# Performance work log

Measured on AMD Instinct MI355X. Metric: run time of the kernel, lower is better.

Reference implementation:

```python
import jax, jax.numpy as jnp
import numpy as np

RADIUS2 = 0.03 ** 2
SIM_THRESH = 0.7
EPS = 1e-8


def setup_inputs() -> dict:
    key = jax.random.key(0)
    k1, k2, k3, k4, k5, k6, k7 = jax.random.split(key, 7)
    B, N, D = 2, 6144, 32
    # points in a 0.3-side cube so radius 0.03 gives realistic neighbor counts
    points = jax.random.uniform(k1, (B, N, 3), dtype=jnp.float32) * 0.3
    embeddings = jax.random.normal(k2, (B, N, D), dtype=jnp.float32)
    leaf_mask = jax.random.randint(k3, (B, N), 0, 2, dtype=jnp.int32)
    # consistency_net: Linear(2D, D) -> ReLU -> Linear(D, D)
    W1 = jax.random.normal(k4, (2 * D, D), dtype=jnp.float32) * (1.0 / np.sqrt(2 * D))
    b1 = jax.random.normal(k5, (D,), dtype=jnp.float32) * 0.01
    W2 = jax.random.normal(k6, (D, D), dtype=jnp.float32) * (1.0 / np.sqrt(D))
    b2 = jax.random.normal(k7, (D,), dtype=jnp.float32) * 0.01
    return {"points": points, "embeddings": embeddings, "leaf_mask": leaf_mask,
            "W1": W1, "b1": b1, "W2": W2, "b2": b2}


def reference(points, embeddings, leaf_mask, W1, b1, W2, b2):
    # points: [B,N,3], embeddings: [B,N,D], leaf_mask: [B,N] int (0/1)
    dt = embeddings.dtype
    leaf = leaf_mask > 0  # [B,N] bool

    # pairwise squared distances via the Gram trick (avoids [B,N,N,3])
    pn = jnp.sum(points * points, axis=-1)                      # [B,N]
    gram = jnp.einsum('bic,bjc->bij', points, points)           # [B,N,N]
    d2 = jnp.maximum(pn[:, :, None] + pn[:, None, :] - 2.0 * gram, 0.0)

    # neighbor mask: within radius AND neighbor is leaf (matches dist<0.03 & leaf_mask)
    nb = (d2 < RADIUS2) & leaf[:, None, :]                      # [B,N,N]

    # cosine similarity with torch's eps clamp on norms
    enorm = jnp.maximum(jnp.linalg.norm(embeddings, axis=-1), EPS)  # [B,N]
    inner = jnp.einsum('bid,bjd->bij', embeddings, embeddings)      # [B,N,N]
    sims = inner / (enorm[:, :, None] * enorm[:, None, :])

    sim_mask = nb & (sims > SIM_THRESH)                          # [B,N,N]
    cnt_nb = jnp.sum(nb, axis=-1)                                # [B,N]
    cnt_sim = jnp.sum(sim_mask, axis=-1)                         # [B,N]

    # mean of similar-neighbor embeddings
    sum_sim = jnp.einsum('bij,bjd->bid', sim_mask.astype(dt), embeddings)
    mean_sim = sum_sim / jnp.maximum(cnt_sim, 1).astype(dt)[..., None]

    # consistency MLP on [center_embedding, mean_similar]
    combined = jnp.concatenate([embeddings, mean_sim], axis=-1)  # [B,N,2D]
    h = jax.nn.relu(jnp.einsum('bnk,kd->bnd', combined, W1) + b1)
    out = jnp.einsum('bnk,kd->bnd', h, W2) + b2                  # [B,N,D]

    # refine only leaf points with >1 neighbor and >0 similar neighbors
    cond = leaf & (cnt_nb > 1) & (cnt_sim > 0)                   # [B,N]
    refined = jnp.where(cond[..., None], out, embeddings)

    # per-batch early exit: sum(leaf_mask) < 10 -> unchanged
    batch_ok = jnp.sum(leaf_mask, axis=-1) >= 10                 # [B]
    return jnp.where(batch_ok[:, None, None], refined, embeddings)
```

## Files before the change

### kernel.cpp

```cpp
#include <hip/hip_runtime.h>

#define NPTS    6144
#define DIM     32
#define NB      2
#define NCELL   1000
#define R2      0.0009f
#define NWAVES  4
#define BLOCK   (NWAVES * 64)
#define LEAFBIT 8192
#define PPT     6
#define NBCAP   128

__device__ __forceinline__ int cellof(float x) {
    int c = (int)(x * (10.0f / 0.3f));
    return min(max(c, 0), 9);
}

#define WS_LEAF   0
#define WS_CSTART 4
#define WS_SORTED 2008

__global__ __launch_bounds__(1024)
void build_cells(const float* __restrict__ points, const int* __restrict__ leaf,
                 int* __restrict__ ws)
{
    __shared__ int s_hist[1024];
    __shared__ int s_cursor[1024];
    __shared__ int s_wsum[16];
    __shared__ int s_leaf;

    const int t = threadIdx.x;
    const int b = blockIdx.x;
    const int w = t >> 6, lane = t & 63;

    s_hist[t] = 0;
    if (t == 0) s_leaf = 0;

    float px[PPT], py[PPT], pz[PPT];
    int   pc[PPT], pw[PPT];

    __syncthreads();

    int lc = 0;
    #pragma unroll
    for (int r = 0; r < PPT; ++r) {
        const int i  = r * 1024 + t;
        const int gi = b * NPTS + i;
        px[r] = points[gi * 3 + 0];
        py[r] = points[gi * 3 + 1];
        pz[r] = points[gi * 3 + 2];
        const int lf = leaf[gi] > 0 ? 1 : 0;
        lc += lf;
        pc[r] = (cellof(pz[r]) * 10 + cellof(py[r])) * 10 + cellof(px[r]);
        pw[r] = i + (lf ? LEAFBIT : 0);
        atomicAdd(&s_hist[pc[r]], 1);
    }
    #pragma unroll
    for (int off = 32; off > 0; off >>= 1) lc += __shfl_down(lc, off);
    if (lane == 0) atomicAdd(&s_leaf, lc);
    __syncthreads();

    const int v = s_hist[t];
    int x = v;
    #pragma unroll
    for (int off = 1; off < 64; off <<= 1) {
        const int y = __shfl_up(x, off);
        if (lane >= off) x += y;
    }
    if (lane == 63) s_wsum[w] = x;
    __syncthreads();
    if (t < 16) {
        int wv = s_wsum[t];
        #pragma unroll
        for (int off = 1; off < 16; off <<= 1) {
            const int y = __shfl_up(wv, off);
            if (t >= off) wv += y;
        }
        s_wsum[t] = wv;
    }
    __syncthreads();
    const int incl = x + (w > 0 ? s_wsum[w - 1] : 0);
    s_cursor[t] = incl - v;

    if (t < NCELL) ws[WS_CSTART + b * (NCELL + 1) + t + 1] = incl;
    if (t == 0) {
        ws[WS_CSTART + b * (NCELL + 1)] = 0;
        ws[WS_LEAF + b] = s_leaf;
    }
    __syncthreads();

    float4* sorted = (float4*)(ws + WS_SORTED) + (size_t)b * NPTS;
    #pragma unroll
    for (int r = 0; r < PPT; ++r) {
        const int pos = atomicAdd(&s_cursor[pc[r]], 1);
        sorted[pos] = make_float4(px[r], py[r], pz[r], (float)pw[r]);
    }
}

__global__ __launch_bounds__(BLOCK)
void refine(const float* __restrict__ emb,
            const float* __restrict__ W1, const float* __restrict__ b1,
            const float* __restrict__ W2, const float* __restrict__ b2,
            const int* __restrict__ ws, float* __restrict__ out)
{
    __shared__ __align__(16) float s_ei[NWAVES][DIM];
    __shared__ float s_mean[NWAVES][DIM];
    __shared__ float s_h[NWAVES][DIM];
    __shared__ int   s_nb[NWAVES][NBCAP];
    __shared__ int   s_sv[NWAVES][NBCAP];

    const int tid  = threadIdx.x;
    const int wid  = tid >> 6;
    const int lane = tid & 63;
    const int s    = blockIdx.x * NWAVES + wid;
    const int b    = s / NPTS;
    const int slot = s - b * NPTS;

    const float4* srt  = (const float4*)(ws + WS_SORTED) + (size_t)b * NPTS;
    const int*    cst  = ws + WS_CSTART + b * (NCELL + 1);
    const float*  embB = emb + (size_t)b * NPTS * DIM;

    const float4 P  = srt[slot];
    const int    iw = (int)P.w;
    const int    io = iw & (LEAFBIT - 1);
    const bool   li = (iw & LEAFBIT) != 0;
    const bool   ok = ws[WS_LEAF + b] >= 10;

    const float4* e4   = (const float4*)(embB + (size_t)io * DIM);
    float4*       out4 = (float4*)(out + ((size_t)b * NPTS + io) * DIM);

    if (!(ok && li)) {
        if (lane < DIM / 4) out4[lane] = e4[lane];
        return;
    }

    if (lane < DIM) s_ei[wid][lane] = ((const float*)e4)[lane];

    float ni2 = 0.0f;
    #pragma unroll
    for (int d = 0; d < DIM; ++d) { const float v = s_ei[wid][d]; ni2 += v * v; }
    const float rni = 1.0f / fmaxf(sqrtf(ni2), 1e-8f);

    const int cx = cellof(P.x), cy = cellof(P.y), cz = cellof(P.z);

    int begv = 0, lenv = 0;
    if (lane < 9) {
        const int z = cz + lane / 3 - 1;
        const int y = cy + lane % 3 - 1;
        if ((unsigned)z <= 9u && (unsigned)y <= 9u) {
            const int rowb = (z * 10 + y) * 10;
            const int c0   = rowb + max(cx - 1, 0);
            const int c1   = rowb + min(cx + 1, 9);
            begv = cst[c0];
            lenv = cst[c1 + 1] - begv;
        }
    }
    const int rb0 = __shfl(begv, 0), rb1 = __shfl(begv, 1), rb2 = __shfl(begv, 2);
    const int rb3 = __shfl(begv, 3), rb4 = __shfl(begv, 4), rb5 = __shfl(begv, 5);
    const int rb6 = __shfl(begv, 6), rb7 = __shfl(begv, 7), rb8 = __shfl(begv, 8);
    const int ln0 = __shfl(lenv, 0), ln1 = __shfl(lenv, 1), ln2 = __shfl(lenv, 2);
    const int ln3 = __shfl(lenv, 3), ln4 = __shfl(lenv, 4), ln5 = __shfl(lenv, 5);
    const int ln6 = __shfl(lenv, 6), ln7 = __shfl(lenv, 7), ln8 = __shfl(lenv, 8);
    const int pf1 = ln0,       pf2 = pf1 + ln1, pf3 = pf2 + ln2;
    const int pf4 = pf3 + ln3, pf5 = pf4 + ln4, pf6 = pf5 + ln5;
    const int pf7 = pf6 + ln6, pf8 = pf7 + ln7, pf9 = pf8 + ln8;

    int nbcnt = 0;
    for (int base = 0; base < pf9; base += 64) {
        const int g = base + lane;
        int j = 0;
        if (g < pf9) j = rb8 + g - pf8;
        if (g < pf8) j = rb7 + g - pf7;
        if (g < pf7) j = rb6 + g - pf6;
        if (g < pf6) j = rb5 + g - pf5;
        if (g < pf5) j = rb4 + g - pf4;
        if (g < pf4) j = rb3 + g - pf3;
        if (g < pf3) j = rb2 + g - pf2;
        if (g < pf2) j = rb1 + g - pf1;
        if (g < pf1) j = rb0 + g;
        const float4 Q  = srt[j];
        const float dx = Q.x - P.x, dy = Q.y - P.y, dz = Q.z - P.z;
        const float d2 = dx * dx + dy * dy + dz * dz;
        const int   jw = (int)Q.w;
        const bool  nb = (g < pf9) && (d2 < R2) && ((jw & LEAFBIT) != 0);
        const unsigned long long m = __ballot(nb);
        if (nb) {
            const int pos = nbcnt + __popcll(m & ((1ull << lane) - 1ull));
            if (pos < NBCAP) s_nb[wid][pos] = jw & (LEAFBIT - 1);
        }
        nbcnt += __popcll(m);
    }
    const int cnt_nb = nbcnt;

    int csim = 0;
    const int nh = min(cnt_nb, NBCAP);
    for (int h0 = 0; h0 < nh; h0 += 64) {
        const int h = h0 + lane;
        bool surv = false;
        int  jo   = 0;
        if (h < nh) {
            jo = s_nb[wid][h];
            const float4* ej4 = (const float4*)(embB + (size_t)jo * DIM);
            float dot = 0.0f, nj2 = 0.0f;
            #pragma unroll
            for (int k = 0; k < DIM / 4; ++k) {
                const float4 v = ej4[k];
                const float4 a = *(const float4*)&s_ei[wid][4 * k];
                dot += a.x * v.x + a.y * v.y + a.z * v.z + a.w * v.w;
                nj2 += v.x * v.x + v.y * v.y + v.z * v.z + v.w * v.w;
            }
            const float rnj = 1.0f / fmaxf(sqrtf(nj2), 1e-8f);
            surv = (dot * rni * rnj) > 0.7f;
        }
        const unsigned long long m = __ballot(surv);
        if (surv) {
            const int pos = csim + __popcll(m & ((1ull << lane) - 1ull));
            s_sv[wid][pos] = jo;
        }
        csim += __popcll(m);
    }

    const bool cond = (cnt_nb > 1) && (csim > 0);

    if (lane < DIM) {
        if (!cond) {
            out[((size_t)b * NPTS + io) * DIM + lane] = s_ei[wid][lane];
        } else {
            float msum = 0.0f;
            for (int v = 0; v < csim; ++v)
                msum += embB[(size_t)s_sv[wid][v] * DIM + lane];
            s_mean[wid][lane] = msum / (float)csim;

            float a0 = b1[lane], a1 = 0.0f;
            #pragma unroll
            for (int k = 0; k < DIM; k += 2) {
                a0 = fmaf(s_ei[wid][k],     W1[k * DIM + lane],       a0);
                a1 = fmaf(s_ei[wid][k + 1], W1[(k + 1) * DIM + lane], a1);
            }
            #pragma unroll
            for (int k = 0; k < DIM; k += 2) {
                a0 = fmaf(s_mean[wid][k],     W1[(DIM + k) * DIM + lane],     a0);
                a1 = fmaf(s_mean[wid][k + 1], W1[(DIM + k + 1) * DIM + lane], a1);
            }
            s_h[wid][lane] = fmaxf(a0 + a1, 0.0f);
            float c0 = b2[lane], c1 = 0.0f;
            #pragma unroll
            for (int k = 0; k < DIM; k += 2) {
                c0 = fmaf(s_h[wid][k],     W2[k * DIM + lane],       c0);
                c1 = fmaf(s_h[wid][k + 1], W2[(k + 1) * DIM + lane], c1);
            }
            out[((size_t)b * NPTS + io) * DIM + lane] = c0 + c1;
        }
    }
}

extern "C" void kernel_launch(void* const* d_in, const int* in_sizes, int n_in,
                              void* d_out, int out_size, void* d_ws, size_t ws_size,
                              hipStream_t stream) {
    const float* points = (const float*)d_in[0];
    const float* emb    = (const float*)d_in[1];
    const int*   leaf   = (const int*)d_in[2];
    const float* W1     = (const float*)d_in[3];
    const float* b1     = (const float*)d_in[4];
    const float* W2     = (const float*)d_in[5];
    const float* b2     = (const float*)d_in[6];
    float*       outp   = (float*)d_out;
    int*         ws     = (int*)d_ws;

    build_cells<<<NB, 1024, 0, stream>>>(points, leaf, ws);

    const int grid = (NB * NPTS) / NWAVES;
    refine<<<grid, BLOCK, 0, stream>>>(emb, W1, b1, W2, b2, ws, outp);
}
```

Before: 88.52 us.

## Index refine by original point order and batch first four candidate chunk loads

The refine kernel now assigns each wave to a point in original order, reading leaf flag and coordinates directly instead of through the cell-sorted array. Output writes become coalesced per block, but adjacent waves no longer share spatial neighborhoods, which reduces cache locality for neighbor gathers. The first four 64-candidate chunks are loaded into registers before any distance tests so several gathers are in flight at once, at the cost of more registers.

```diff
diff --git a/kernel.cpp b/kernel.cpp
--- a/kernel.cpp
+++ b/kernel.cpp
@@ -97,8 +97,23 @@
     }
 }
 
+#define RUN_SELECT(g, j)                                                      \
+    {                                                                         \
+        j = 0;                                                                \
+        if ((g) < pf9) j = rb8 + (g) - pf8;                                   \
+        if ((g) < pf8) j = rb7 + (g) - pf7;                                   \
+        if ((g) < pf7) j = rb6 + (g) - pf6;                                   \
+        if ((g) < pf6) j = rb5 + (g) - pf5;                                   \
+        if ((g) < pf5) j = rb4 + (g) - pf4;                                   \
+        if ((g) < pf4) j = rb3 + (g) - pf3;                                   \
+        if ((g) < pf3) j = rb2 + (g) - pf2;                                   \
+        if ((g) < pf2) j = rb1 + (g) - pf1;                                   \
+        if ((g) < pf1) j = rb0 + (g);                                         \
+    }
+
 __global__ __launch_bounds__(BLOCK)
 void refine(const float* __restrict__ emb,
+            const float* __restrict__ points, const int* __restrict__ leaf,
             const float* __restrict__ W1, const float* __restrict__ b1,
             const float* __restrict__ W2, const float* __restrict__ b2,
             const int* __restrict__ ws, float* __restrict__ out)
@@ -114,34 +129,34 @@
     const int lane = tid & 63;
     const int s    = blockIdx.x * NWAVES + wid;
     const int b    = s / NPTS;
-    const int slot = s - b * NPTS;
+
+    const bool li = leaf[s] > 0;
+    const bool ok = ws[WS_LEAF + b] >= 10;
+
+    const float4* e4   = (const float4*)(emb + (size_t)s * DIM);
+    float4*       out4 = (float4*)(out + (size_t)s * DIM);
+
+    if (!(ok && li)) {
+        if (lane < DIM / 4) out4[lane] = e4[lane];
+        return;
+    }
+
+    const float pix = points[s * 3 + 0];
+    const float piy = points[s * 3 + 1];
+    const float piz = points[s * 3 + 2];
+
+    if (lane < DIM) s_ei[wid][lane] = ((const float*)e4)[lane];
 
     const float4* srt  = (const float4*)(ws + WS_SORTED) + (size_t)b * NPTS;
     const int*    cst  = ws + WS_CSTART + b * (NCELL + 1);
     const float*  embB = emb + (size_t)b * NPTS * DIM;
 
-    const float4 P  = srt[slot];
-    const int    iw = (int)P.w;
-    const int    io = iw & (LEAFBIT - 1);
-    const bool   li = (iw & LEAFBIT) != 0;
-    const bool   ok = ws[WS_LEAF + b] >= 10;
-
-    const float4* e4   = (const float4*)(embB + (size_t)io * DIM);
-    float4*       out4 = (float4*)(out + ((size_t)b * NPTS + io) * DIM);
-
-    if (!(ok && li)) {
-        if (lane < DIM / 4) out4[lane] = e4[lane];
-        return;
-    }
-
-    if (lane < DIM) s_ei[wid][lane] = ((const float*)e4)[lane];
-
     float ni2 = 0.0f;
     #pragma unroll
     for (int d = 0; d < DIM; ++d) { const float v = s_ei[wid][d]; ni2 += v * v; }
     const float rni = 1.0f / fmaxf(sqrtf(ni2), 1e-8f);
 
-    const int cx = cellof(P.x), cy = cellof(P.y), cz = cellof(P.z);
+    const int cx = cellof(pix), cy = cellof(piy), cz = cellof(piz);
 
     int begv = 0, lenv = 0;
     if (lane < 9) {
@@ -165,30 +180,50 @@
     const int pf4 = pf3 + ln3, pf5 = pf4 + ln4, pf6 = pf5 + ln5;
     const int pf7 = pf6 + ln6, pf8 = pf7 + ln7, pf9 = pf8 + ln8;
 
+    const int nch = (pf9 + 63) >> 6;
     int nbcnt = 0;
-    for (int base = 0; base < pf9; base += 64) {
-        const int g = base + lane;
-        int j = 0;
-        if (g < pf9) j = rb8 + g - pf8;
-        if (g < pf8) j = rb7 + g - pf7;
-        if (g < pf7) j = rb6 + g - pf6;
-        if (g < pf6) j = rb5 + g - pf5;
-        if (g < pf5) j = rb4 + g - pf4;
-        if (g < pf4) j = rb3 + g - pf3;
-        if (g < pf3) j = rb2 + g - pf2;
-        if (g < pf2) j = rb1 + g - pf1;
-        if (g < pf1) j = rb0 + g;
-        const float4 Q  = srt[j];
-        const float dx = Q.x - P.x, dy = Q.y - P.y, dz = Q.z - P.z;
-        const float d2 = dx * dx + dy * dy + dz * dz;
-        const int   jw = (int)Q.w;
-        const bool  nb = (g < pf9) && (d2 < R2) && ((jw & LEAFBIT) != 0);
-        const unsigned long long m = __ballot(nb);
-        if (nb) {
-            const int pos = nbcnt + __popcll(m & ((1ull << lane) - 1ull));
-            if (pos < NBCAP) s_nb[wid][pos] = jw & (LEAFBIT - 1);
-        }
-        nbcnt += __popcll(m);
+    {
+        float4 Q[4];
+        const int nb4 = min(nch, 4);
+        #pragma unroll
+        for (int c = 0; c < 4; ++c) {
+            if (c < nb4) {
+                const int g = c * 64 + lane;
+                int j; RUN_SELECT(g, j);
+                Q[c] = srt[j];
+            }
+        }
+        #pragma unroll
+        for (int c = 0; c < 4; ++c) {
+            if (c < nb4) {
+                const int g  = c * 64 + lane;
+                const float dx = Q[c].x - pix, dy = Q[c].y - piy, dz = Q[c].z - piz;
+                const float d2 = dx * dx + dy * dy + dz * dz;
+                const int   jw = (int)Q[c].w;
+                const bool  nb = (g < pf9) && (d2 < R2) && ((jw & LEAFBIT) != 0);
+                const unsigned long long m = __ballot(nb);
+                if (nb) {
+                    const int pos = nbcnt + __popcll(m & ((1ull << lane) - 1ull));
+                    if (pos < NBCAP) s_nb[wid][pos] = jw & (LEAFBIT - 1);
+                }
+                nbcnt += __popcll(m);
+            }
+        }
+        for (int base = 256; base < pf9; base += 64) {
+            const int g = base + lane;
+            int j; RUN_SELECT(g, j);
+            const float4 Qf = srt[j];
+            const float dx = Qf.x - pix, dy = Qf.y - piy, dz = Qf.z - piz;
+            const float d2 = dx * dx + dy * dy + dz * dz;
+            const int   jw = (int)Qf.w;
+            const bool  nb = (g < pf9) && (d2 < R2) && ((jw & LEAFBIT) != 0);
+            const unsigned long long m = __ballot(nb);
+            if (nb) {
+                const int pos = nbcnt + __popcll(m & ((1ull << lane) - 1ull));
+                if (pos < NBCAP) s_nb[wid][pos] = jw & (LEAFBIT - 1);
+            }
+            nbcnt += __popcll(m);
+        }
     }
     const int cnt_nb = nbcnt;
 
@@ -224,7 +259,7 @@
 
     if (lane < DIM) {
         if (!cond) {
-            out[((size_t)b * NPTS + io) * DIM + lane] = s_ei[wid][lane];
+            out[(size_t)s * DIM + lane] = s_ei[wid][lane];
         } else {
             float msum = 0.0f;
             for (int v = 0; v < csim; ++v)
@@ -249,7 +284,7 @@
                 c0 = fmaf(s_h[wid][k],     W2[k * DIM + lane],       c0);
                 c1 = fmaf(s_h[wid][k + 1], W2[(k + 1) * DIM + lane], c1);
             }
-            out[((size_t)b * NPTS + io) * DIM + lane] = c0 + c1;
+            out[(size_t)s * DIM + lane] = c0 + c1;
         }
     }
 }
@@ -270,5 +305,5 @@
     build_cells<<<NB, 1024, 0, stream>>>(points, leaf, ws);
 
     const int grid = (NB * NPTS) / NWAVES;
-    refine<<<grid, BLOCK, 0, stream>>>(emb, W1, b1, W2, b2, ws, outp);
+    refine<<<grid, BLOCK, 0, stream>>>(emb, points, leaf, W1, b1, W2, b2, ws, outp);
 }
```

Result: no change. 90.29 us (+2.0%).

## Split cell-binning into parallel histogram, scan and scatter kernels

Applied to the files above, without the earlier changes.

Replaces the single two-block build_cells kernel with three kernels: per-chunk histograms over 16 blocks, a per-batch scan that produces per-chunk cursor bases, and a 16-block scatter. The aim is to spread the binning work across more compute units instead of serialising it on two blocks. In exchange it adds two extra kernel launches and global-memory round trips for the partial histograms.

```diff
diff --git a/kernel.cpp b/kernel.cpp
--- a/kernel.cpp
+++ b/kernel.cpp
@@ -8,8 +8,9 @@
 #define NWAVES  4
 #define BLOCK   (NWAVES * 64)
 #define LEAFBIT 8192
-#define PPT     6
 #define NBCAP   128
+#define HBLK    8
+#define HPTS    (NPTS / HBLK)
 
 __device__ __forceinline__ int cellof(float x) {
     int c = (int)(x * (10.0f / 0.3f));
@@ -19,49 +20,73 @@
 #define WS_LEAF   0
 #define WS_CSTART 4
 #define WS_SORTED 2008
-
-__global__ __launch_bounds__(1024)
-void build_cells(const float* __restrict__ points, const int* __restrict__ leaf,
-                 int* __restrict__ ws)
+#define WS_PH     51160
+#define WS_PLEAF  67544
+#define WS_PBS    67560
+
+__global__ __launch_bounds__(256)
+void hist16(const float* __restrict__ points, const int* __restrict__ leaf,
+            int* __restrict__ ws)
 {
     __shared__ int s_hist[1024];
-    __shared__ int s_cursor[1024];
+    __shared__ int s_lc;
+
+    const int t  = threadIdx.x;
+    const int bk = blockIdx.x;
+    const int b  = bk >> 3;
+    const int lb = bk & 7;
+
+    #pragma unroll
+    for (int c = t; c < 1024; c += 256) s_hist[c] = 0;
+    if (t == 0) s_lc = 0;
+    __syncthreads();
+
+    int lc = 0;
+    #pragma unroll
+    for (int r = 0; r < 3; ++r) {
+        const int i  = lb * HPTS + r * 256 + t;
+        const int gi = b * NPTS + i;
+        const float x = points[gi * 3 + 0];
+        const float y = points[gi * 3 + 1];
+        const float z = points[gi * 3 + 2];
+        const int cell = (cellof(z) * 10 + cellof(y)) * 10 + cellof(x);
+        atomicAdd(&s_hist[cell], 1);
+        lc += (leaf[gi] > 0) ? 1 : 0;
+    }
+    #pragma unroll
+    for (int off = 32; off > 0; off >>= 1) lc += __shfl_down(lc, off);
+    if ((t & 63) == 0) atomicAdd(&s_lc, lc);
+    __syncthreads();
+
+    #pragma unroll
+    for (int c = t; c < 1024; c += 256)
+        ws[WS_PH + bk * 1024 + c] = s_hist[c];
+    if (t == 0) ws[WS_PLEAF + bk] = s_lc;
+}
+
+__global__ __launch_bounds__(1024)
+void scan2(int* __restrict__ ws)
+{
     __shared__ int s_wsum[16];
-    __shared__ int s_leaf;
 
     const int t = threadIdx.x;
     const int b = blockIdx.x;
     const int w = t >> 6, lane = t & 63;
 
-    s_hist[t] = 0;
-    if (t == 0) s_leaf = 0;
-
-    float px[PPT], py[PPT], pz[PPT];
-    int   pc[PPT], pw[PPT];
-
-    __syncthreads();
-
-    int lc = 0;
-    #pragma unroll
-    for (int r = 0; r < PPT; ++r) {
-        const int i  = r * 1024 + t;
-        const int gi = b * NPTS + i;
-        px[r] = points[gi * 3 + 0];
-        py[r] = points[gi * 3 + 1];
-        pz[r] = points[gi * 3 + 2];
-        const int lf = leaf[gi] > 0 ? 1 : 0;
-        lc += lf;
-        pc[r] = (cellof(pz[r]) * 10 + cellof(py[r])) * 10 + cellof(px[r]);
-        pw[r] = i + (lf ? LEAFBIT : 0);
-        atomicAdd(&s_hist[pc[r]], 1);
-    }
-    #pragma unroll
-    for (int off = 32; off > 0; off >>= 1) lc += __shfl_down(lc, off);
-    if (lane == 0) atomicAdd(&s_leaf, lc);
-    __syncthreads();
-
-    const int v = s_hist[t];
-    int x = v;
+    int p[HBLK];
+    int total = 0;
+    if (t < NCELL) {
+        #pragma unroll
+        for (int k = 0; k < HBLK; ++k) {
+            p[k] = ws[WS_PH + (b * HBLK + k) * 1024 + t];
+            total += p[k];
+        }
+    } else {
+        #pragma unroll
+        for (int k = 0; k < HBLK; ++k) p[k] = 0;
+    }
+
+    int x = total;
     #pragma unroll
     for (int off = 1; off < 64; off <<= 1) {
         const int y = __shfl_up(x, off);
@@ -80,20 +105,55 @@
     }
     __syncthreads();
     const int incl = x + (w > 0 ? s_wsum[w - 1] : 0);
-    s_cursor[t] = incl - v;
-
-    if (t < NCELL) ws[WS_CSTART + b * (NCELL + 1) + t + 1] = incl;
-    if (t == 0) {
-        ws[WS_CSTART + b * (NCELL + 1)] = 0;
-        ws[WS_LEAF + b] = s_leaf;
-    }
+    const int excl = incl - total;
+
+    if (t < NCELL) {
+        ws[WS_CSTART + b * (NCELL + 1) + t + 1] = incl;
+        int run = excl;
+        #pragma unroll
+        for (int k = 0; k < HBLK; ++k) {
+            ws[WS_PBS + (b * HBLK + k) * 1024 + t] = run;
+            run += p[k];
+        }
+    }
+    if (t == 0) ws[WS_CSTART + b * (NCELL + 1)] = 0;
+
+    if (w == 0) {
+        int v = (lane < HBLK) ? ws[WS_PLEAF + b * HBLK + lane] : 0;
+        #pragma unroll
+        for (int off = 4; off > 0; off >>= 1) v += __shfl_down(v, off);
+        if (lane == 0) ws[WS_LEAF + b] = v;
+    }
+}
+
+__global__ __launch_bounds__(256)
+void scatter16(const float* __restrict__ points, const int* __restrict__ leaf,
+               int* __restrict__ ws)
+{
+    __shared__ int s_cur[1024];
+
+    const int t  = threadIdx.x;
+    const int bk = blockIdx.x;
+    const int b  = bk >> 3;
+    const int lb = bk & 7;
+
+    #pragma unroll
+    for (int c = t; c < 1024; c += 256)
+        s_cur[c] = ws[WS_PBS + bk * 1024 + c];
     __syncthreads();
 
     float4* sorted = (float4*)(ws + WS_SORTED) + (size_t)b * NPTS;
     #pragma unroll
-    for (int r = 0; r < PPT; ++r) {
-        const int pos = atomicAdd(&s_cursor[pc[r]], 1);
-        sorted[pos] = make_float4(px[r], py[r], pz[r], (float)pw[r]);
+    for (int r = 0; r < 3; ++r) {
+        const int i  = lb * HPTS + r * 256 + t;
+        const int gi = b * NPTS + i;
+        const float x = points[gi * 3 + 0];
+        const float y = points[gi * 3 + 1];
+        const float z = points[gi * 3 + 2];
+        const int cell = (cellof(z) * 10 + cellof(y)) * 10 + cellof(x);
+        const int pos  = atomicAdd(&s_cur[cell], 1);
+        const float w4 = (float)(i + (leaf[gi] > 0 ? LEAFBIT : 0));
+        sorted[pos] = make_float4(x, y, z, w4);
     }
 }
 
@@ -267,7 +327,9 @@
     float*       outp   = (float*)d_out;
     int*         ws     = (int*)d_ws;
 
-    build_cells<<<NB, 1024, 0, stream>>>(points, leaf, ws);
+    hist16   <<<NB * HBLK, 256,  0, stream>>>(points, leaf, ws);
+    scan2    <<<NB,        1024, 0, stream>>>(ws);
+    scatter16<<<NB * HBLK, 256,  0, stream>>>(points, leaf, ws);
 
     const int grid = (NB * NPTS) / NWAVES;
     refine<<<grid, BLOCK, 0, stream>>>(emb, W1, b1, W2, b2, ws, outp);
```

Result: no change. 89.45 us (+1.0%).
